# Performance work log

Measured on AMD Instinct MI355X. Metric: run time of the kernel, lower is better.

## Reference

```python
import jax, jax.numpy as jnp
import numpy as np

DIM = 1024
HEAD_DIM = 64
NUM_HEADS = DIM // HEAD_DIM
SCALE = HEAD_DIM ** -0.5


def setup_inputs() -> dict:
    key = jax.random.key(0)
    ks = jax.random.split(key, 12)
    b, n = 4, 2048
    std = DIM ** -0.5
    inp = {
        'words': jax.random.normal(ks[0], (b, n, DIM), jnp.float32),
        'position': jax.random.normal(ks[1], (b, n, DIM), jnp.float32),
        'conscious': jax.random.normal(ks[2], (b, n, DIM), jnp.float32),
        # projection weights stored as [in, out] (torch Linear W^T)
        'w_wq': jax.random.normal(ks[3], (DIM, DIM), jnp.float32) * std,
        'w_wk': jax.random.normal(ks[4], (DIM, DIM), jnp.float32) * std,
        'w_wv': jax.random.normal(ks[5], (DIM, DIM), jnp.float32) * std,
        'w_pq': jax.random.normal(ks[6], (DIM, DIM), jnp.float32) * std,
        'w_pk': jax.random.normal(ks[7], (DIM, DIM), jnp.float32) * std,
        'w_cq': jax.random.normal(ks[8], (DIM, DIM), jnp.float32) * std,
        'w_ck': jax.random.normal(ks[9], (DIM, DIM), jnp.float32) * std,
        'w_out': jax.random.normal(ks[10], (DIM, DIM), jnp.float32) * std,
        'b_out': jax.random.normal(ks[11], (DIM,), jnp.float32) * 0.01,
    }
    return inp


def _heads(x):
    b, n, _ = x.shape
    return x.reshape(b, n, NUM_HEADS, HEAD_DIM).transpose(0, 2, 1, 3)  # b h n d


def reference(words, position, conscious, w_wq, w_wk, w_wv, w_pq, w_pk, w_cq, w_ck, w_out, b_out):
    # fused multi-source q/k: sum of three projections per source
    q = _heads(words @ w_wq + position @ w_pq + conscious @ w_cq)
    k = _heads(words @ w_wk + position @ w_pk + conscious @ w_ck)
    v = _heads(words @ w_wv)
    sim = jnp.einsum('bhid,bhjd->bhij', q, k) * SCALE
    attn = jax.nn.softmax(sim, axis=-1)
    out = jnp.einsum('bhij,bhjd->bhid', attn, v)
    b, h, n, d = out.shape
    out = out.transpose(0, 2, 1, 3).reshape(b, n, h * d)
    return out @ w_out + b_out
```

## Files before the change

### kernel.cpp

```cpp
#include <hip/hip_runtime.h>
#include <hip/hip_bf16.h>

typedef __bf16 bf16_t;
typedef __attribute__((ext_vector_type(8))) __bf16 bf16x8;
typedef __attribute__((ext_vector_type(4))) float f32x4;
typedef __attribute__((ext_vector_type(16))) float f32x16;

__device__ __forceinline__ void gld_lds16(const void* g, void* l) {
  __builtin_amdgcn_global_load_lds((const __attribute__((address_space(1))) void*)g,
                                   (__attribute__((address_space(3))) void*)l, 16, 0, 0);
}

__global__ __launch_bounds__(256) void prep_kernel(
    const float* __restrict__ w, const float* __restrict__ p,
    const float* __restrict__ c,
    const float* __restrict__ w_wq, const float* __restrict__ w_pq,
    const float* __restrict__ w_cq, const float* __restrict__ w_wk,
    const float* __restrict__ w_pk, const float* __restrict__ w_ck,
    const float* __restrict__ w_wv, const float* __restrict__ w_out,
    bf16_t* __restrict__ X, bf16_t* __restrict__ Wqkt,
    bf16_t* __restrict__ Wvt, bf16_t* __restrict__ Wot)
{
  __shared__ float t[32][33];
  const int bid = blockIdx.x, tid = threadIdx.x;
  if (bid < 24576) {
    unsigned idx = bid * 256u + tid;
    unsigned src = idx >> 21;
    unsigned rem = idx & ((1u << 21) - 1);
    unsigned row = rem >> 8;
    unsigned k4  = (rem & 255u) * 4u;
    const float* s = (src == 0) ? w : (src == 1) ? p : c;
    f32x4 v = *(const f32x4*)(s + (size_t)row * 1024 + k4);
    ushort4 u;
    u.x = __builtin_bit_cast(unsigned short, (bf16_t)v[0]);
    u.y = __builtin_bit_cast(unsigned short, (bf16_t)v[1]);
    u.z = __builtin_bit_cast(unsigned short, (bf16_t)v[2]);
    u.w = __builtin_bit_cast(unsigned short, (bf16_t)v[3]);
    *(ushort4*)(X + (size_t)row * 3072 + src * 1024 + k4) = u;
  } else {
    const int tb = bid - 24576;
    const int z = tb >> 10, rem = tb & 1023;
    const int by = rem >> 5, bx = rem & 31;
    const int tx = tid & 31, ty = tid >> 5;
    const float* src; bf16_t* dst; int dstride, koff, roff;
    switch (z) {
      case 0: src = w_wq;  dst = Wqkt; dstride = 3072; koff = 0;    roff = 0;    break;
      case 1: src = w_pq;  dst = Wqkt; dstride = 3072; koff = 1024; roff = 0;    break;
      case 2: src = w_cq;  dst = Wqkt; dstride = 3072; koff = 2048; roff = 0;    break;
      case 3: src = w_wk;  dst = Wqkt; dstride = 3072; koff = 0;    roff = 1024; break;
      case 4: src = w_pk;  dst = Wqkt; dstride = 3072; koff = 1024; roff = 1024; break;
      case 5: src = w_ck;  dst = Wqkt; dstride = 3072; koff = 2048; roff = 1024; break;
      case 6: src = w_wv;  dst = Wvt;  dstride = 1024; koff = 0;    roff = 0;    break;
      default: src = w_out; dst = Wot; dstride = 1024; koff = 0;    roff = 0;    break;
    }
    int x = bx * 32 + tx;
    int y0 = by * 32;
    for (int i = ty; i < 32; i += 8)
      t[i][tx] = src[(size_t)(y0 + i) * 1024 + x];
    __syncthreads();
    int n0 = bx * 32;
    for (int i = ty; i < 32; i += 8)
      dst[(size_t)(n0 + i + roff) * dstride + koff + y0 + tx] = (bf16_t)t[tx][i];
  }
}

__global__ __launch_bounds__(512, 2) void gemm256_qk(
    const bf16_t* __restrict__ A, int lda,
    const bf16_t* __restrict__ Bt, int K,
    bf16_t* __restrict__ Qo, bf16_t* __restrict__ Ko, float scale, int nbx)
{
  __shared__ bf16_t As[2][256 * 64];
  __shared__ bf16_t Bs[2][256 * 64];

  const int tid = threadIdx.x;
  const int wave = tid >> 6, lane = tid & 63;
  const int wm = wave >> 2, wn = wave & 3;
  const int lrow = lane & 15, lch = lane >> 4;

  const int nwg = gridDim.x, cpx = nwg >> 3;
  const int id  = blockIdx.x;
  const int swz = (id & 7) * cpx + (id >> 3);
  const int mb = swz / nbx, nb = swz % nbx;
  const int m0 = mb * 256, n0 = nb * 256;

  const int srow = tid >> 3, spp = tid & 7;

  auto STAGE_A = [&](int buf, int k0, int h) {
#pragma unroll
    for (int i = 0; i < 2; ++i) {
      int r = h * 128 + i * 64 + srow;
      int gsw = (spp ^ (r & 7)) * 8;
      gld_lds16(A + (size_t)(m0 + r) * lda + k0 + gsw, &As[buf][r * 64 + spp * 8]);
    }
  };
  auto STAGE_B = [&](int buf, int k0, int h) {
#pragma unroll
    for (int i = 0; i < 2; ++i) {
      int r = h * 128 + i * 64 + srow;
      int gsw = (spp ^ (r & 7)) * 8;
      gld_lds16(Bt + (size_t)(n0 + r) * K + k0 + gsw, &Bs[buf][r * 64 + spp * 8]);
    }
  };

  const int NT = K >> 6;
  STAGE_A(0, 0, 0); STAGE_A(0, 0, 1);
  STAGE_B(0, 0, 0); STAGE_B(0, 0, 1);
  STAGE_B(1, 64, 0); STAGE_B(1, 64, 1);
  asm volatile("s_waitcnt vmcnt(4)" ::: "memory");
  asm volatile("s_barrier" ::: "memory");

  f32x4 acc[8][4] = {};

  for (int kt = 0; kt < NT; ++kt) {
    const int cur = kt & 1, nxt = cur ^ 1;
    bf16x8 bfr[4][2];

#pragma unroll
    for (int p = 0; p < 4; ++p) {
      bf16x8 af[2][2];
#pragma unroll
      for (int j = 0; j < 2; ++j)
#pragma unroll
        for (int ks = 0; ks < 2; ++ks) {
          int r = wm * 128 + (p * 2 + j) * 16 + lrow;
          af[j][ks] = *(const bf16x8*)&As[cur][r * 64 + (((ks * 4 + lch) ^ (r & 7)) * 8)];
        }
      if (p == 0) {
#pragma unroll
        for (int n = 0; n < 4; ++n)
#pragma unroll
          for (int ks = 0; ks < 2; ++ks) {
            int r = wn * 64 + n * 16 + lrow;
            bfr[n][ks] = *(const bf16x8*)&Bs[cur][r * 64 + (((ks * 4 + lch) ^ (r & 7)) * 8)];
          }
      }
      if (p == 0 && kt + 1 < NT) STAGE_A(nxt, (kt + 1) * 64, 0);
      if (p == 1 && kt + 1 < NT) STAGE_A(nxt, (kt + 1) * 64, 1);
      if (p == 2 && kt + 2 < NT) STAGE_B(cur, (kt + 2) * 64, 0);
      if (p == 3 && kt + 2 < NT) STAGE_B(cur, (kt + 2) * 64, 1);
      if (p == 3) {
        if (kt + 2 < NT)      asm volatile("s_waitcnt vmcnt(4)" ::: "memory");
        else                  asm volatile("s_waitcnt vmcnt(0)" ::: "memory");
      }
      asm volatile("s_barrier" ::: "memory");
      __builtin_amdgcn_s_setprio(1);
#pragma unroll
      for (int ks = 0; ks < 2; ++ks)
#pragma unroll
        for (int j = 0; j < 2; ++j)
#pragma unroll
          for (int n = 0; n < 4; ++n)
            acc[p * 2 + j][n] = __builtin_amdgcn_mfma_f32_16x16x32_bf16(
                af[j][ks], bfr[n][ks], acc[p * 2 + j][n], 0, 0, 0);
      __builtin_amdgcn_s_setprio(0);
      if (p == 3)
        asm volatile("s_barrier" ::: "memory");
    }
  }

  const int g = lane >> 4, cl = lane & 15;
#pragma unroll
  for (int m = 0; m < 8; ++m) {
    int m_base = m0 + wm * 128 + m * 16 + g * 4;
    int bb = m_base >> 11, nn = m_base & 2047;
#pragma unroll
    for (int n = 0; n < 4; ++n) {
      int col = n0 + wn * 64 + n * 16 + cl;
      bf16_t* dst = (col < 1024) ? Qo : Ko;
      int cc2 = col & 1023;
      float sc = (col < 1024) ? scale : 1.0f;
      int h = cc2 >> 6, d = cc2 & 63;
      size_t base = ((size_t)(bb * 16 + h) * 2048 + nn) * 64 + d;
#pragma unroll
      for (int r = 0; r < 4; ++r)
        dst[base + (size_t)r * 64] = (bf16_t)(acc[m][n][r] * sc);
    }
  }
}

template<int EPI>
__global__ __launch_bounds__(512, 2) void gemm128x256(
    const bf16_t* __restrict__ A, int lda,
    const bf16_t* __restrict__ Bt, int K,
    void* __restrict__ Cout, const float* __restrict__ bias)
{
  __shared__ bf16_t As[2][128 * 64];
  __shared__ bf16_t Bs[2][256 * 64];

  const int tid = threadIdx.x;
  const int wave = tid >> 6, lane = tid & 63;
  const int wm = wave >> 2, wn = wave & 3;
  const int lrow = lane & 15, lch = lane >> 4;

  const int nwg = gridDim.x, cpx = nwg >> 3;
  const int id  = blockIdx.x;
  const int swz = (id & 7) * cpx + (id >> 3);
  const int mb = swz >> 2, nb = swz & 3;
  const int m0 = mb * 128, n0 = nb * 256;

  const int srow = tid >> 3, spp = tid & 7;

  auto STAGE_A = [&](int buf, int k0, int h) {
    int r = h * 64 + srow;
    int gsw = (spp ^ (r & 7)) * 8;
    gld_lds16(A + (size_t)(m0 + r) * lda + k0 + gsw, &As[buf][r * 64 + spp * 8]);
  };
  auto STAGE_B = [&](int buf, int k0, int h) {
#pragma unroll
    for (int i = 0; i < 2; ++i) {
      int r = h * 128 + i * 64 + srow;
      int gsw = (spp ^ (r & 7)) * 8;
      gld_lds16(Bt + (size_t)(n0 + r) * K + k0 + gsw, &Bs[buf][r * 64 + spp * 8]);
    }
  };

  const int NT = K >> 6;
  STAGE_A(0, 0, 0); STAGE_A(0, 0, 1);
  STAGE_B(0, 0, 0); STAGE_B(0, 0, 1);
  STAGE_B(1, 64, 0); STAGE_B(1, 64, 1);
  asm volatile("s_waitcnt vmcnt(4)" ::: "memory");
  asm volatile("s_barrier" ::: "memory");

  f32x4 acc[4][4] = {};

  for (int kt = 0; kt < NT; ++kt) {
    const int cur = kt & 1, nxt = cur ^ 1;
    bf16x8 bfr[4][2];

#pragma unroll
    for (int p = 0; p < 2; ++p) {
      bf16x8 af[2][2];
#pragma unroll
      for (int j = 0; j < 2; ++j)
#pragma unroll
        for (int ks = 0; ks < 2; ++ks) {
          int r = wm * 64 + (p * 2 + j) * 16 + lrow;
          af[j][ks] = *(const bf16x8*)&As[cur][r * 64 + (((ks * 4 + lch) ^ (r & 7)) * 8)];
        }
      if (p == 0) {
#pragma unroll
        for (int n = 0; n < 4; ++n)
#pragma unroll
          for (int ks = 0; ks < 2; ++ks) {
            int r = wn * 64 + n * 16 + lrow;
            bfr[n][ks] = *(const bf16x8*)&Bs[cur][r * 64 + (((ks * 4 + lch) ^ (r & 7)) * 8)];
          }
      }
      if (p == 0 && kt + 1 < NT) { STAGE_A(nxt, (kt + 1) * 64, 0); STAGE_A(nxt, (kt + 1) * 64, 1); }
      if (p == 1 && kt + 2 < NT) { STAGE_B(cur, (kt + 2) * 64, 0); STAGE_B(cur, (kt + 2) * 64, 1); }
      if (p == 1) {
        if (kt + 2 < NT)      asm volatile("s_waitcnt vmcnt(4)" ::: "memory");
        else                  asm volatile("s_waitcnt vmcnt(0)" ::: "memory");
      }
      asm volatile("s_barrier" ::: "memory");
      __builtin_amdgcn_s_setprio(1);
#pragma unroll
      for (int ks = 0; ks < 2; ++ks)
#pragma unroll
        for (int j = 0; j < 2; ++j)
#pragma unroll
          for (int n = 0; n < 4; ++n)
            acc[p * 2 + j][n] = __builtin_amdgcn_mfma_f32_16x16x32_bf16(
                af[j][ks], bfr[n][ks], acc[p * 2 + j][n], 0, 0, 0);
      __builtin_amdgcn_s_setprio(0);
      asm volatile("s_barrier" ::: "memory");
    }
  }

  const int g = lane >> 4, cl = lane & 15;
  if (EPI == 1) {
    bf16_t* Vo = (bf16_t*)Cout;
#pragma unroll
    for (int m = 0; m < 4; ++m) {
      int m_base = m0 + wm * 64 + m * 16 + g * 4;
      int bb = m_base >> 11, nn = m_base & 2047;
#pragma unroll
      for (int n = 0; n < 4; ++n) {
        int col = n0 + wn * 64 + n * 16 + cl;
        int h = col >> 6, d = col & 63;
        ushort4 u;
        u.x = __builtin_bit_cast(unsigned short, (bf16_t)acc[m][n][0]);
        u.y = __builtin_bit_cast(unsigned short, (bf16_t)acc[m][n][1]);
        u.z = __builtin_bit_cast(unsigned short, (bf16_t)acc[m][n][2]);
        u.w = __builtin_bit_cast(unsigned short, (bf16_t)acc[m][n][3]);
        *(ushort4*)(Vo + ((size_t)(bb * 16 + h) * 64 + d) * 2048 + nn) = u;
      }
    }
  } else {
    float* Co = (float*)Cout;
#pragma unroll
    for (int m = 0; m < 4; ++m) {
      int m_base = m0 + wm * 64 + m * 16 + g * 4;
#pragma unroll
      for (int n = 0; n < 4; ++n) {
        int col = n0 + wn * 64 + n * 16 + cl;
        float bv = bias[col];
#pragma unroll
        for (int r = 0; r < 4; ++r)
          Co[(size_t)(m_base + r) * 1024 + col] = acc[m][n][r] + bv;
      }
    }
  }
}

__global__ __launch_bounds__(256, 2) void attn_kernel(
    const bf16_t* __restrict__ Q, const bf16_t* __restrict__ Kb,
    const bf16_t* __restrict__ Vt, bf16_t* __restrict__ O)
{
  __shared__ bf16_t Ks[2][64 * 64];
  __shared__ bf16_t Vs[2][64 * 64];

  const int fid = blockIdx.x;
  const int swz = (fid & 7) * 64 + (fid >> 3);
  const int bh = swz >> 3, qt = swz & 7;
  const int bb = bh >> 4, h = bh & 15;

  const int tid = threadIdx.x, wave = tid >> 6, lane = tid & 63;
  const int lq = lane & 31;
  const int lh = lane >> 5;

  const bf16_t* Qb    = Q  + ((size_t)bh * 2048 + qt * 256) * 64;
  const bf16_t* Kbase = Kb + (size_t)bh * 2048 * 64;
  const bf16_t* Vbase = Vt + (size_t)bh * 64 * 2048;

  const int srow = tid >> 3, spp = tid & 7;

  auto STAGE_K = [&](int buf, int tile) {
#pragma unroll
    for (int i = 0; i < 2; ++i) {
      int r = i * 32 + srow;
      int sg = (spp ^ (r & 7)) * 8;
      gld_lds16(Kbase + (size_t)(tile * 64 + r) * 64 + sg, &Ks[buf][i * 2048 + tid * 8]);
    }
  };
  auto STAGE_V = [&](int buf, int tile) {
#pragma unroll
    for (int i = 0; i < 2; ++i) {
      int r = i * 32 + srow;
      int sg = (spp ^ (r & 7)) * 8;
      gld_lds16(Vbase + (size_t)r * 2048 + tile * 64 + sg, &Vs[buf][i * 2048 + tid * 8]);
    }
  };

  STAGE_K(0, 0); STAGE_V(0, 0); STAGE_K(1, 1);

  bf16x8 qf0[4], qf1[4];
#pragma unroll
  for (int kf = 0; kf < 4; ++kf) {
    qf0[kf] = *(const bf16x8*)(Qb + (size_t)(wave * 64 + lq) * 64 + kf * 16 + lh * 8);
    qf1[kf] = *(const bf16x8*)(Qb + (size_t)(wave * 64 + 32 + lq) * 64 + kf * 16 + lh * 8);
  }

  f32x16 acc0[2] = {}, acc1[2] = {};
  float m0r = -1.0e30f, l0r = 0.f, m1r = -1.0e30f, l1r = 0.f;
  bf16x8 pb0[4], pb1[4];

  auto QKT2 = [&](int tile, f32x16 (&s0)[2], f32x16 (&s1)[2]) {
    const int kb = tile & 1;
#pragma unroll
    for (int nb2 = 0; nb2 < 2; ++nb2) {
      int r = nb2 * 32 + lq;
      f32x16 z0 = {}, z1 = {};
#pragma unroll
      for (int kf = 0; kf < 4; ++kf) {
        bf16x8 ka = *(const bf16x8*)&Ks[kb][r * 64 + (((kf * 2 + lh) ^ (r & 7)) * 8)];
        z0 = __builtin_amdgcn_mfma_f32_32x32x16_bf16(ka, qf0[kf], z0, 0, 0, 0);
        z1 = __builtin_amdgcn_mfma_f32_32x32x16_bf16(ka, qf1[kf], z1, 0, 0, 0);
      }
      s0[nb2] = z0; s1[nb2] = z1;
    }
  };

  auto PV2 = [&](int tile) {
    const int vb = tile & 1;
#pragma unroll
    for (int ks = 0; ks < 4; ++ks)
#pragma unroll
      for (int db = 0; db < 2; ++db) {
        int r = db * 32 + lq;
        bf16x8 va = *(const bf16x8*)&Vs[vb][r * 64 + (((ks * 2 + lh) ^ (r & 7)) * 8)];
        acc0[db] = __builtin_amdgcn_mfma_f32_32x32x16_bf16(va, pb0[ks], acc0[db], 0, 0, 0);
        acc1[db] = __builtin_amdgcn_mfma_f32_32x32x16_bf16(va, pb1[ks], acc1[db], 0, 0, 0);
      }
  };

  auto SOFTMAX = [&](f32x16 (&st)[2], float& mr, float& lr,
                     f32x16 (&ac)[2], bf16x8 (&po)[4]) {
    float tmax = fmaxf(st[0][0], st[0][1]);
#pragma unroll
    for (int nb2 = 0; nb2 < 2; ++nb2)
#pragma unroll
      for (int rg = (nb2 ? 0 : 2); rg < 16; rg += 2)
        tmax = fmaxf(fmaxf(tmax, st[nb2][rg]), st[nb2][rg + 1]);
    tmax = fmaxf(tmax, __shfl_xor(tmax, 32));

    if (!__all(tmax <= mr + 8.0f)) {
      float mnew = fmaxf(mr, tmax);
      float corr = __builtin_amdgcn_exp2f(mr - mnew);
      mr = mnew;
      lr *= corr;
#pragma unroll
      for (int db = 0; db < 2; ++db)
#pragma unroll
        for (int rg = 0; rg < 16; ++rg)
          ac[db][rg] *= corr;
    }

    float sm = 0.f;
#pragma unroll
    for (int nb2 = 0; nb2 < 2; ++nb2)
#pragma unroll
      for (int rg = 0; rg < 16; ++rg) {
        float p = __builtin_amdgcn_exp2f(st[nb2][rg] - mr);
        st[nb2][rg] = p;
        sm += p;
      }
    lr += sm;

#pragma unroll
    for (int ks = 0; ks < 4; ++ks) {
      const int nb2 = ks >> 1;
      const int R = (ks & 1) * 8;
      unsigned x0, x1, y0, y1;
      asm("v_cvt_pk_bf16_f32 %0, %1, %2" : "=v"(x0) : "v"(st[nb2][R + 0]), "v"(st[nb2][R + 1]));
      asm("v_cvt_pk_bf16_f32 %0, %1, %2" : "=v"(x1) : "v"(st[nb2][R + 2]), "v"(st[nb2][R + 3]));
      asm("v_cvt_pk_bf16_f32 %0, %1, %2" : "=v"(y0) : "v"(st[nb2][R + 4]), "v"(st[nb2][R + 5]));
      asm("v_cvt_pk_bf16_f32 %0, %1, %2" : "=v"(y1) : "v"(st[nb2][R + 6]), "v"(st[nb2][R + 7]));
      asm volatile("v_permlane32_swap_b32 %0, %1" : "+v"(x0), "+v"(y0));
      asm volatile("v_permlane32_swap_b32 %0, %1" : "+v"(x1), "+v"(y1));
      int4 pw;
      pw.x = (int)x0; pw.y = (int)x1; pw.z = (int)y0; pw.w = (int)y1;
      po[ks] = __builtin_bit_cast(bf16x8, pw);
    }
  };

  asm volatile("s_waitcnt vmcnt(0)" ::: "memory");
  __builtin_amdgcn_s_barrier();
  asm volatile("" ::: "memory");
  {
    f32x16 s0[2], s1[2];
    QKT2(0, s0, s1);
    SOFTMAX(s0, m0r, l0r, acc0, pb0);
    SOFTMAX(s1, m1r, l1r, acc1, pb1);
  }
  asm volatile("s_waitcnt lgkmcnt(0)" ::: "memory");
  __builtin_amdgcn_s_barrier();
  asm volatile("" ::: "memory");

  for (int t = 0; t < 32; ++t) {
    if (t < 30)       { STAGE_V((t + 1) & 1, t + 1); STAGE_K(t & 1, t + 2); }
    else if (t == 30) { STAGE_V(1, 31); }
    if (t < 30)       asm volatile("s_waitcnt vmcnt(4)" ::: "memory");
    else if (t == 30) asm volatile("s_waitcnt vmcnt(2)" ::: "memory");
    else              asm volatile("s_waitcnt vmcnt(0)" ::: "memory");
    __builtin_amdgcn_s_barrier();
    asm volatile("" ::: "memory");

    f32x16 s0[2], s1[2];
    __builtin_amdgcn_s_setprio(1);
    if (t < 31) QKT2(t + 1, s0, s1);
    PV2(t);
    __builtin_amdgcn_s_setprio(0);
    if (t < 31) {
      SOFTMAX(s0, m0r, l0r, acc0, pb0);
      SOFTMAX(s1, m1r, l1r, acc1, pb1);
    }

    asm volatile("s_waitcnt lgkmcnt(0)" ::: "memory");
    __builtin_amdgcn_s_barrier();
    asm volatile("" ::: "memory");
  }

  float l0t = l0r + __shfl_xor(l0r, 32);
  float l1t = l1r + __shfl_xor(l1r, 32);
  float inv0 = 1.0f / l0t, inv1 = 1.0f / l1t;
#pragma unroll
  for (int qb = 0; qb < 2; ++qb) {
    float inv = qb ? inv1 : inv0;
    int nn = qt * 256 + wave * 64 + qb * 32 + lq;
    size_t obase = ((size_t)bb * 2048 + nn) * 1024 + h * 64;
#pragma unroll
    for (int db = 0; db < 2; ++db)
#pragma unroll
      for (int rr = 0; rr < 4; ++rr) {
        f32x16& a = qb ? acc1[db] : acc0[db];
        ushort4 u;
        u.x = __builtin_bit_cast(unsigned short, (bf16_t)(a[rr * 4 + 0] * inv));
        u.y = __builtin_bit_cast(unsigned short, (bf16_t)(a[rr * 4 + 1] * inv));
        u.z = __builtin_bit_cast(unsigned short, (bf16_t)(a[rr * 4 + 2] * inv));
        u.w = __builtin_bit_cast(unsigned short, (bf16_t)(a[rr * 4 + 3] * inv));
        *(ushort4*)(O + obase + db * 32 + rr * 8 + lh * 4) = u;
      }
  }
}

extern "C" void kernel_launch(void* const* d_in, const int* in_sizes, int n_in,
                              void* d_out, int out_size, void* d_ws, size_t ws_size,
                              hipStream_t stream) {
  const float* words     = (const float*)d_in[0];
  const float* position  = (const float*)d_in[1];
  const float* conscious = (const float*)d_in[2];
  const float* w_wq  = (const float*)d_in[3];
  const float* w_wk  = (const float*)d_in[4];
  const float* w_wv  = (const float*)d_in[5];
  const float* w_pq  = (const float*)d_in[6];
  const float* w_pk  = (const float*)d_in[7];
  const float* w_cq  = (const float*)d_in[8];
  const float* w_ck  = (const float*)d_in[9];
  const float* w_out = (const float*)d_in[10];
  const float* b_out = (const float*)d_in[11];

  char* ws = (char*)d_ws;
  bf16_t* Xcat = (bf16_t*)(ws);
  bf16_t* Wqkt = (bf16_t*)(ws + 50331648);
  bf16_t* Wvt  = (bf16_t*)(ws + 62914560);
  bf16_t* Wot  = (bf16_t*)(ws + 65011712);
  bf16_t* Qb   = (bf16_t*)(ws + 67108864);
  bf16_t* Kbf  = (bf16_t*)(ws + 83886080);
  bf16_t* Vtb  = (bf16_t*)(ws + 100663296);
  bf16_t* Ob   = (bf16_t*)(ws + 117440512);

  prep_kernel<<<32768, 256, 0, stream>>>(words, position, conscious,
      w_wq, w_pq, w_cq, w_wk, w_pk, w_ck, w_wv, w_out, Xcat, Wqkt, Wvt, Wot);

  gemm256_qk<<<256, 512, 0, stream>>>(Xcat, 3072, Wqkt, 3072, Qb, Kbf,
                                      0.125f * 1.44269504f, 8);
  gemm128x256<1><<<256, 512, 0, stream>>>(Xcat, 3072, Wvt, 1024, Vtb, nullptr);

  attn_kernel<<<512, 256, 0, stream>>>(Qb, Kbf, Vtb, Ob);

  gemm128x256<2><<<256, 512, 0, stream>>>(Ob, 1024, Wot, 1024, (float*)d_out, b_out);
}
```

Measured before the change: 265.2 us.

## Split attention KV range in two halves and merge with log-sum-exp combine

```diff
diff --git a/kernel.cpp b/kernel.cpp
--- a/kernel.cpp
+++ b/kernel.cpp
@@ -305,15 +305,17 @@
 
 __global__ __launch_bounds__(256, 2) void attn_kernel(
     const bf16_t* __restrict__ Q, const bf16_t* __restrict__ Kb,
-    const bf16_t* __restrict__ Vt, bf16_t* __restrict__ O)
+    const bf16_t* __restrict__ Vt, bf16_t* __restrict__ Opart,
+    float* __restrict__ ML)
 {
   __shared__ bf16_t Ks[2][64 * 64];
   __shared__ bf16_t Vs[2][64 * 64];
 
   const int fid = blockIdx.x;
-  const int swz = (fid & 7) * 64 + (fid >> 3);
-  const int bh = swz >> 3, qt = swz & 7;
-  const int bb = bh >> 4, h = bh & 15;
+  const int swz = (fid & 7) * 128 + (fid >> 3);
+  const int bh = swz >> 4, rest = swz & 15;
+  const int qt = rest >> 1, half = rest & 1;
+  const int T0 = half * 16;
 
   const int tid = threadIdx.x, wave = tid >> 6, lane = tid & 63;
   const int lq = lane & 31;
@@ -325,24 +327,24 @@
 
   const int srow = tid >> 3, spp = tid & 7;
 
-  auto STAGE_K = [&](int buf, int tile) {
+  auto STAGE_K = [&](int buf, int gt) {
 #pragma unroll
     for (int i = 0; i < 2; ++i) {
       int r = i * 32 + srow;
       int sg = (spp ^ (r & 7)) * 8;
-      gld_lds16(Kbase + (size_t)(tile * 64 + r) * 64 + sg, &Ks[buf][i * 2048 + tid * 8]);
-    }
-  };
-  auto STAGE_V = [&](int buf, int tile) {
+      gld_lds16(Kbase + (size_t)(gt * 64 + r) * 64 + sg, &Ks[buf][i * 2048 + tid * 8]);
+    }
+  };
+  auto STAGE_V = [&](int buf, int gt) {
 #pragma unroll
     for (int i = 0; i < 2; ++i) {
       int r = i * 32 + srow;
       int sg = (spp ^ (r & 7)) * 8;
-      gld_lds16(Vbase + (size_t)r * 2048 + tile * 64 + sg, &Vs[buf][i * 2048 + tid * 8]);
-    }
-  };
-
-  STAGE_K(0, 0); STAGE_V(0, 0); STAGE_K(1, 1);
+      gld_lds16(Vbase + (size_t)r * 2048 + gt * 64 + sg, &Vs[buf][i * 2048 + tid * 8]);
+    }
+  };
+
+  STAGE_K(0, T0); STAGE_V(0, T0); STAGE_K(1, T0 + 1);
 
   bf16x8 qf0[4], qf1[4];
 #pragma unroll
@@ -355,8 +357,8 @@
   float m0r = -1.0e30f, l0r = 0.f, m1r = -1.0e30f, l1r = 0.f;
   bf16x8 pb0[4], pb1[4];
 
-  auto QKT2 = [&](int tile, f32x16 (&s0)[2], f32x16 (&s1)[2]) {
-    const int kb = tile & 1;
+  auto QKT2 = [&](int t, f32x16 (&s0)[2], f32x16 (&s1)[2]) {
+    const int kb = t & 1;
 #pragma unroll
     for (int nb2 = 0; nb2 < 2; ++nb2) {
       int r = nb2 * 32 + lq;
@@ -371,8 +373,8 @@
     }
   };
 
-  auto PV2 = [&](int tile) {
-    const int vb = tile & 1;
+  auto PV2 = [&](int t) {
+    const int vb = t & 1;
 #pragma unroll
     for (int ks = 0; ks < 4; ++ks)
 #pragma unroll
@@ -447,21 +449,21 @@
   __builtin_amdgcn_s_barrier();
   asm volatile("" ::: "memory");
 
-  for (int t = 0; t < 32; ++t) {
-    if (t < 30)       { STAGE_V((t + 1) & 1, t + 1); STAGE_K(t & 1, t + 2); }
-    else if (t == 30) { STAGE_V(1, 31); }
-    if (t < 30)       asm volatile("s_waitcnt vmcnt(4)" ::: "memory");
-    else if (t == 30) asm volatile("s_waitcnt vmcnt(2)" ::: "memory");
+  for (int t = 0; t < 16; ++t) {
+    if (t < 14)       { STAGE_V((t + 1) & 1, T0 + t + 1); STAGE_K(t & 1, T0 + t + 2); }
+    else if (t == 14) { STAGE_V(1, T0 + 15); }
+    if (t < 14)       asm volatile("s_waitcnt vmcnt(4)" ::: "memory");
+    else if (t == 14) asm volatile("s_waitcnt vmcnt(2)" ::: "memory");
     else              asm volatile("s_waitcnt vmcnt(0)" ::: "memory");
     __builtin_amdgcn_s_barrier();
     asm volatile("" ::: "memory");
 
     f32x16 s0[2], s1[2];
     __builtin_amdgcn_s_setprio(1);
-    if (t < 31) QKT2(t + 1, s0, s1);
+    if (t < 15) QKT2(t + 1, s0, s1);
     PV2(t);
     __builtin_amdgcn_s_setprio(0);
-    if (t < 31) {
+    if (t < 15) {
       SOFTMAX(s0, m0r, l0r, acc0, pb0);
       SOFTMAX(s1, m1r, l1r, acc1, pb1);
     }
@@ -474,11 +476,12 @@
   float l0t = l0r + __shfl_xor(l0r, 32);
   float l1t = l1r + __shfl_xor(l1r, 32);
   float inv0 = 1.0f / l0t, inv1 = 1.0f / l1t;
+  const size_t rbase = (size_t)bh * 2048 + qt * 256 + wave * 64;
+  bf16_t* Op = Opart + (size_t)half * 8388608 + rbase * 64;
 #pragma unroll
   for (int qb = 0; qb < 2; ++qb) {
     float inv = qb ? inv1 : inv0;
-    int nn = qt * 256 + wave * 64 + qb * 32 + lq;
-    size_t obase = ((size_t)bb * 2048 + nn) * 1024 + h * 64;
+    int nn_loc = qb * 32 + lq;
 #pragma unroll
     for (int db = 0; db < 2; ++db)
 #pragma unroll
@@ -489,9 +492,36 @@
         u.y = __builtin_bit_cast(unsigned short, (bf16_t)(a[rr * 4 + 1] * inv));
         u.z = __builtin_bit_cast(unsigned short, (bf16_t)(a[rr * 4 + 2] * inv));
         u.w = __builtin_bit_cast(unsigned short, (bf16_t)(a[rr * 4 + 3] * inv));
-        *(ushort4*)(O + obase + db * 32 + rr * 8 + lh * 4) = u;
-      }
-  }
+        *(ushort4*)(Op + (size_t)nn_loc * 64 + db * 32 + rr * 8 + lh * 4) = u;
+      }
+  }
+  if (lh == 0) {
+    float* MLh = ML + (size_t)half * 131072 + rbase;
+    MLh[lq]      = m0r + log2f(l0t);
+    MLh[32 + lq] = m1r + log2f(l1t);
+  }
+}
+
+__global__ __launch_bounds__(256) void combine_kernel(
+    const bf16_t* __restrict__ Opart, const float* __restrict__ ML,
+    bf16_t* __restrict__ O)
+{
+  int gid = blockIdx.x * 256 + threadIdx.x;
+  int row = gid >> 3, dseg = (gid & 7) * 8;
+  float lseA = ML[row], lseB = ML[131072 + row];
+  float M = fmaxf(lseA, lseB);
+  float wA = __builtin_amdgcn_exp2f(lseA - M);
+  float wB = __builtin_amdgcn_exp2f(lseB - M);
+  float inv = 1.0f / (wA + wB);
+  wA *= inv; wB *= inv;
+  bf16x8 va = *(const bf16x8*)(Opart + (size_t)row * 64 + dseg);
+  bf16x8 vb = *(const bf16x8*)(Opart + 8388608 + (size_t)row * 64 + dseg);
+  bf16x8 vo;
+#pragma unroll
+  for (int i = 0; i < 8; ++i)
+    vo[i] = (bf16_t)(wA * (float)va[i] + wB * (float)vb[i]);
+  int bh = row >> 11, q = row & 2047, bb = bh >> 4, hh = bh & 15;
+  *(bf16x8*)(O + ((size_t)(bb * 2048 + q)) * 1024 + hh * 64 + dseg) = vo;
 }
 
 extern "C" void kernel_launch(void* const* d_in, const int* in_sizes, int n_in,
@@ -519,6 +549,8 @@
   bf16_t* Kbf  = (bf16_t*)(ws + 83886080);
   bf16_t* Vtb  = (bf16_t*)(ws + 100663296);
   bf16_t* Ob   = (bf16_t*)(ws + 117440512);
+  bf16_t* Opart = (bf16_t*)(ws);
+  float*  ML    = (float*)(ws + 33554432);
 
   prep_kernel<<<32768, 256, 0, stream>>>(words, position, conscious,
       w_wq, w_pq, w_cq, w_wk, w_pk, w_ck, w_wv, w_out, Xcat, Wqkt, Wvt, Wot);
@@ -527,7 +559,8 @@
                                       0.125f * 1.44269504f, 8);
   gemm128x256<1><<<256, 512, 0, stream>>>(Xcat, 3072, Wvt, 1024, Vtb, nullptr);
 
-  attn_kernel<<<512, 256, 0, stream>>>(Qb, Kbf, Vtb, Ob);
+  attn_kernel<<<1024, 256, 0, stream>>>(Qb, Kbf, Vtb, Opart, ML);
+  combine_kernel<<<4096, 256, 0, stream>>>(Opart, ML, Ob);
 
   gemm128x256<2><<<256, 512, 0, stream>>>(Ob, 1024, Wot, 1024, (float*)d_out, b_out);
 }
```

Measured after the change: 278.6 us. 5.0% more time.
